# Performance work log

Measured on AMD Instinct MI355X. Metric: run time of the kernel, lower is better.

## Reference

```python
import jax, jax.numpy as jnp
import numpy as np

N = 262144          # ray samples
L = 16              # grid levels
T = 2 ** 19         # hash table entries per level
F = 2               # features per entry
NMIN, NMAX = 16, 2048
SB = 1.0            # scene_bound
DW, CW = 64, 64     # density / color MLP widths

_PRIMES = jnp.array([1, 2654435761, 805459861], dtype=jnp.uint32)
_OFFS = jnp.asarray(np.stack(np.meshgrid([0, 1], [0, 1], [0, 1], indexing='ij'), -1).reshape(8, 3), dtype=jnp.uint32)  # 8 cube corners


def _scalings():
    g = np.exp((np.log(NMAX) - np.log(NMIN)) / (L - 1))
    return jnp.asarray(np.floor(NMIN * g ** np.arange(L)), dtype=jnp.float32)  # (L,)


def hash_encode(pos01, table):
    # pos01: (N,3) in [0,1]; table: (L*T, F)
    scaled = pos01[:, None, :] * _scalings()[None, :, None]        # (N,L,3)
    floor = jnp.floor(scaled)
    frac = scaled - floor                                          # (N,L,3)
    corners = floor.astype(jnp.uint32)[:, :, None, :] + _OFFS[None, None]  # (N,L,8,3)
    h = corners * _PRIMES                                          # uint32 wraparound hashing
    idx = (h[..., 0] ^ h[..., 1] ^ h[..., 2]) % jnp.uint32(T)      # (N,L,8)
    idx = idx.astype(jnp.int32) + (jnp.arange(L, dtype=jnp.int32) * T)[None, :, None]
    feats = table[idx]                                             # (N,L,8,F) gather
    sel = _OFFS.astype(bool)[None, None]                           # (1,1,8,3)
    w = jnp.prod(jnp.where(sel, frac[:, :, None, :], 1.0 - frac[:, :, None, :]), axis=-1)  # (N,L,8)
    out = jnp.einsum('nlcf,nlc->nlf', feats, w)                    # trilinear interp
    return out.reshape(out.shape[0], L * F)                        # (N, 32)


def sh_encode(d):
    # 4th-order real spherical harmonics, 16 components (instant-ngp convention)
    x, y, z = d[..., 0], d[..., 1], d[..., 2]
    xx, yy, zz = x * x, y * y, z * z
    xy, yz, xz = x * y, y * z, x * z
    return jnp.stack([
        jnp.full_like(x, 0.28209479177387814),
        -0.48860251190291987 * y,
        0.48860251190291987 * z,
        -0.48860251190291987 * x,
        1.0925484305920792 * xy,
        -1.0925484305920792 * yz,
        0.94617469575755997 * zz - 0.31539156525252005,
        -1.0925484305920792 * xz,
        0.54627421529603959 * (xx - yy),
        0.59004358992664352 * y * (-3.0 * xx + yy),
        2.8906114426405538 * xy * z,
        0.45704579946446572 * y * (1.0 - 5.0 * zz),
        0.3731763325901154 * z * (5.0 * zz - 3.0),
        0.45704579946446572 * x * (1.0 - 5.0 * zz),
        1.445305721320277 * z * (xx - yy),
        0.59004358992664352 * x * (xx - 3.0 * yy),
    ], axis=-1)  # (N,16)


def setup_inputs() -> dict:
    key = jax.random.key(0)
    ks = jax.random.split(key, 10)
    position = jax.random.uniform(ks[0], (N, 3), jnp.float32, -SB, SB)
    d = jax.random.normal(ks[1], (N, 3), jnp.float32)
    direction = d / jnp.linalg.norm(d, axis=-1, keepdims=True)
    hash_table = jax.random.uniform(ks[2], (L * T, F), jnp.float32, -1e-4, 1e-4)
    def dense(k, fin, fout, std):
        return (jax.random.normal(k, (fin, fout), jnp.float32) * std,
                jnp.zeros((fout,), jnp.float32))
    w1, b1 = dense(ks[3], L * F, DW, 0.01)      # normal() init in source
    w2, b2 = dense(ks[4], DW, 16, 0.01)
    w3, b3 = dense(ks[5], 16 + 16, CW, 0.01)
    w4, b4 = dense(ks[6], CW, CW, 0.01)
    w5, b5 = dense(ks[7], CW, 3, 0.1)           # default lecun-ish scale
    return dict(position=position, direction=direction, hash_table=hash_table,
                w1=w1, b1=b1, w2=w2, b2=b2, w3=w3, b3=b3, w4=w4, b4=b4, w5=w5, b5=b5)


def reference(position, direction, hash_table, w1, b1, w2, b2, w3, b3, w4, b4, w5, b5):
    p = (position + SB) / (2.0 * SB)                 # -> [0,1]
    enc = hash_encode(p, hash_table)                 # (N,32)
    h = jax.nn.relu(enc @ w1 + b1)                   # density MLP
    h = h @ w2 + b2                                  # (N,16)
    density = jnp.exp(h[:, 0:1])                     # exponential_density_activation
    sh = sh_encode(direction)                        # (N,16)
    c = jnp.concatenate([h, sh], axis=-1)            # (N,32)
    c = jax.nn.relu(c @ w3 + b3)
    c = jax.nn.relu(c @ w4 + b4)
    c = c @ w5 + b5
    color = jax.nn.sigmoid(c)                        # high_dynamic_range=False
    return jnp.concatenate([density, color], axis=-1)  # (N,4) drgbs
```

## Files before the change

kernel.cpp:

```cpp
#include <hip/hip_runtime.h>
#include <cmath>

namespace {
constexpr int kN = 262144;
constexpr int kL = 16;
constexpr int kT = 1 << 19;
constexpr unsigned kTMask = kT - 1;
constexpr int kB = 4096;

typedef __attribute__((ext_vector_type(8))) short short8;
typedef __attribute__((ext_vector_type(4))) float f32x4;
typedef __attribute__((ext_vector_type(4))) unsigned short ushort4v;

struct Scales { float s[kL]; };

__device__ __forceinline__ unsigned short f2bf(float f) {
    unsigned u = __builtin_bit_cast(unsigned, f);
    return (unsigned short)((u + 0x7FFFu + ((u >> 16) & 1u)) >> 16);
}

__global__ __launch_bounds__(256) void prep_w(
    const float* __restrict__ w1, const float* __restrict__ w2,
    const float* __restrict__ w3, const float* __restrict__ w4,
    const float* __restrict__ w5, unsigned short* __restrict__ out)
{
    const int i = blockIdx.x * 256 + threadIdx.x;
    const int f = i >> 9;
    const int l = (i >> 3) & 63;
    const int e = i & 7;
    const int cl = l & 15;
    const int kg = l >> 4;
    float v = 0.0f;
    if (f < 4) {
        v = w1[(kg * 8 + e) * 64 + f * 16 + cl];
    } else if (f < 6) {
        const int q = f - 4;
        v = w2[(q * 32 + kg * 8 + e) * 16 + cl];
    } else if (f < 10) {
        v = w3[(kg * 8 + e) * 64 + (f - 6) * 16 + cl];
    } else if (f < 18) {
        const int g = f - 10, q = g >> 2, nt = g & 3;
        v = w4[(q * 32 + kg * 8 + e) * 64 + nt * 16 + cl];
    } else {
        const int q = f - 18;
        v = (cl < 3) ? w5[(q * 32 + kg * 8 + e) * 3 + cl] : 0.0f;
    }
    out[i] = f2bf(v);
}

__global__ __launch_bounds__(256) void bucket_hist(
    const float* __restrict__ pos,
    unsigned short* __restrict__ key,
    unsigned* __restrict__ hist)
{
    const int n = blockIdx.x * 256 + threadIdx.x;
    const float px = (pos[n * 3 + 0] + 1.0f) * 0.5f;
    const float py = (pos[n * 3 + 1] + 1.0f) * 0.5f;
    const float pz = (pos[n * 3 + 2] + 1.0f) * 0.5f;
    const int cx = min(15, (int)(px * 16.0f));
    const int cy = min(15, (int)(py * 16.0f));
    const int cz = min(15, (int)(pz * 16.0f));
    const int k = (cx << 8) | (cy << 4) | cz;
    key[n] = (unsigned short)k;
    atomicAdd(&hist[k], 1u);
}

__global__ __launch_bounds__(1024) void bucket_scan(
    const unsigned* __restrict__ hist,
    unsigned* __restrict__ cursor)
{
    __shared__ unsigned s[1024];
    const int t = threadIdx.x;
    const unsigned v0 = hist[4 * t], v1 = hist[4 * t + 1];
    const unsigned v2 = hist[4 * t + 2], v3 = hist[4 * t + 3];
    const unsigned a0 = v0, a1 = a0 + v1, a2 = a1 + v2, a3 = a2 + v3;
    s[t] = a3;
    __syncthreads();
    for (int off = 1; off < 1024; off <<= 1) {
        unsigned x = 0;
        if (t >= off) x = s[t - off];
        __syncthreads();
        if (t >= off) s[t] += x;
        __syncthreads();
    }
    const unsigned base = (t > 0) ? s[t - 1] : 0u;
    cursor[4 * t]     = base;
    cursor[4 * t + 1] = base + a0;
    cursor[4 * t + 2] = base + a1;
    cursor[4 * t + 3] = base + a2;
}

__global__ __launch_bounds__(256) void bucket_scatter(
    const float* __restrict__ pos, const float* __restrict__ dir,
    const unsigned short* __restrict__ key,
    unsigned* __restrict__ cursor,
    float* __restrict__ spos, float* __restrict__ sdir,
    unsigned* __restrict__ s2o)
{
    const int n = blockIdx.x * 256 + threadIdx.x;
    const unsigned k = key[n];
    const unsigned i = atomicAdd(&cursor[k], 1u);
    s2o[i] = (unsigned)n;
    spos[i * 3 + 0] = pos[n * 3 + 0];
    spos[i * 3 + 1] = pos[n * 3 + 1];
    spos[i * 3 + 2] = pos[n * 3 + 2];
    sdir[i * 3 + 0] = dir[n * 3 + 0];
    sdir[i * 3 + 1] = dir[n * 3 + 1];
    sdir[i * 3 + 2] = dir[n * 3 + 2];
}

__global__ __launch_bounds__(256) void ngp_encode(
    const float* __restrict__ spos,
    const float2* __restrict__ table,
    unsigned* __restrict__ enc,
    Scales sc)
{
    const int bid = blockIdx.x;
    const int l = bid >> 10;
    const int n = ((bid & 1023) << 8) | threadIdx.x;

    const float s = sc.s[l];
    const float2* __restrict__ tl = table + (size_t)l * kT;

    const float px = (spos[n * 3 + 0] + 1.0f) * 0.5f;
    const float py = (spos[n * 3 + 1] + 1.0f) * 0.5f;
    const float pz = (spos[n * 3 + 2] + 1.0f) * 0.5f;
    const float sx = px * s, sy = py * s, sz = pz * s;
    const float fx = floorf(sx), fy = floorf(sy), fz = floorf(sz);
    const float rx = sx - fx, ry = sy - fy, rz = sz - fz;
    const unsigned cx = (unsigned)fx, cy = (unsigned)fy, cz = (unsigned)fz;

    const unsigned hy0 = cy * 2654435761u, hy1 = (cy + 1u) * 2654435761u;
    const unsigned hz0 = cz * 805459861u,  hz1 = (cz + 1u) * 805459861u;

    float4 pr[4];
    float2 ex[4];
    unsigned idx0v[4], hyzv[4];

    #pragma unroll
    for (int j = 0; j < 4; ++j) {
        const unsigned hyz = ((j >> 1) ? hy1 : hy0) ^ ((j & 1) ? hz1 : hz0);
        hyzv[j] = hyz;
        const unsigned idx0 = (cx ^ hyz) & kTMask;
        idx0v[j] = idx0;
        pr[j] = *reinterpret_cast<const float4*>(tl + (idx0 & ~1u));
    }

    if (cx & 1u) {
        const unsigned cx1 = cx + 1u;
        #pragma unroll
        for (int j = 0; j < 4; ++j)
            ex[j] = tl[(cx1 ^ hyzv[j]) & kTMask];
    }

    const bool odd = (cx & 1u) != 0u;
    const float wx0 = 1.0f - rx, wx1 = rx;
    float f0 = 0.f, f1 = 0.f;
    #pragma unroll
    for (int j = 0; j < 4; ++j) {
        const float wyz = ((j >> 1) ? ry : 1.0f - ry) *
                          ((j & 1) ? rz : 1.0f - rz);
        const bool hi = (idx0v[j] & 1u) != 0u;
        const float c0x = hi ? pr[j].z : pr[j].x;
        const float c0y = hi ? pr[j].w : pr[j].y;
        const float c1x = odd ? ex[j].x : (hi ? pr[j].x : pr[j].z);
        const float c1y = odd ? ex[j].y : (hi ? pr[j].y : pr[j].w);
        f0 = fmaf(c0x, wx0 * wyz, f0);
        f1 = fmaf(c0y, wx0 * wyz, f1);
        f0 = fmaf(c1x, wx1 * wyz, f0);
        f1 = fmaf(c1y, wx1 * wyz, f1);
    }
    enc[(size_t)l * kN + n] = (unsigned)f2bf(f0) | ((unsigned)f2bf(f1) << 16);
}

__global__ __launch_bounds__(256) void ngp_mlp_mfma(
    const unsigned* __restrict__ enc,
    const unsigned short* __restrict__ wbf,
    const float* __restrict__ sdir,
    const unsigned* __restrict__ s2o,
    const float* __restrict__ b1, const float* __restrict__ b2,
    const float* __restrict__ b3, const float* __restrict__ b4,
    const float* __restrict__ b5,
    float* __restrict__ out)
{
    __shared__ unsigned short sA[4][4096];
    __shared__ unsigned short sB[4][2048];

    const int tid = threadIdx.x;
    const int wid = tid >> 6;
    const int l   = tid & 63;
    const int cl  = l & 15;
    const int kg  = l >> 4;
    unsigned short* __restrict__ A_ = sA[wid];
    unsigned short* __restrict__ B_ = sB[wid];
    const int gbase = blockIdx.x * 256 + wid * 64;

    {
        const int s = gbase + l;
        const float x = sdir[s * 3 + 0], y = sdir[s * 3 + 1], z = sdir[s * 3 + 2];
        const float xx = x * x, yy = y * y, zz = z * z;
        const float xy = x * y, yz = y * z, xz = x * z;
        float sh[16];
        sh[0] = 0.28209479177387814f;
        sh[1] = -0.48860251190291987f * y;
        sh[2] = 0.48860251190291987f * z;
        sh[3] = -0.48860251190291987f * x;
        sh[4] = 1.0925484305920792f * xy;
        sh[5] = -1.0925484305920792f * yz;
        sh[6] = 0.94617469575755997f * zz - 0.31539156525252005f;
        sh[7] = -1.0925484305920792f * xz;
        sh[8] = 0.54627421529603959f * (xx - yy);
        sh[9] = 0.59004358992664352f * y * (-3.0f * xx + yy);
        sh[10] = 2.8906114426405538f * xy * z;
        sh[11] = 0.45704579946446572f * y * (1.0f - 5.0f * zz);
        sh[12] = 0.3731763325901154f * z * (5.0f * zz - 3.0f);
        sh[13] = 0.45704579946446572f * x * (1.0f - 5.0f * zz);
        sh[14] = 1.445305721320277f * z * (xx - yy);
        sh[15] = 0.59004358992664352f * x * (xx - 3.0f * yy);
        #pragma unroll
        for (int j = 0; j < 16; ++j)
            B_[(l >> 4) * 512 + (16 + j) * 16 + (l & 15)] = f2bf(sh[j]);
    }

    short8 A1[4];
    #pragma unroll
    for (int m = 0; m < 4; ++m) {
        #pragma unroll
        for (int j = 0; j < 4; ++j) {
            const unsigned v = enc[(size_t)(kg * 4 + j) * kN + (gbase + m * 16 + cl)];
            A1[m][2 * j]     = (short)(v & 0xFFFFu);
            A1[m][2 * j + 1] = (short)(v >> 16);
        }
    }
    {
        short8 B1[4];
        #pragma unroll
        for (int nt = 0; nt < 4; ++nt)
            B1[nt] = *reinterpret_cast<const short8*>(&wbf[(size_t)(nt) * 512 + l * 8]);

        f32x4 acc[4][4];
        #pragma unroll
        for (int nt = 0; nt < 4; ++nt) {
            const float bv = b1[nt * 16 + cl];
            #pragma unroll
            for (int m = 0; m < 4; ++m) {
                acc[m][nt][0] = bv; acc[m][nt][1] = bv; acc[m][nt][2] = bv; acc[m][nt][3] = bv;
            }
        }
        #pragma unroll
        for (int m = 0; m < 4; ++m)
            #pragma unroll
            for (int nt = 0; nt < 4; ++nt)
                acc[m][nt] = __builtin_amdgcn_mfma_f32_16x16x32_bf16(A1[m], B1[nt], acc[m][nt], 0, 0, 0);

        #pragma unroll
        for (int m = 0; m < 4; ++m) {
            #pragma unroll
            for (int nt = 0; nt < 4; ++nt) {
                ushort4v pk;
                #pragma unroll
                for (int r = 0; r < 4; ++r) pk[r] = f2bf(fmaxf(acc[m][nt][r], 0.0f));
                *reinterpret_cast<ushort4v*>(&A_[m * 1024 + (nt * 16 + cl) * 16 + kg * 4]) = pk;
            }
        }
    }

    {
        short8 A2[4][2];
        #pragma unroll
        for (int m = 0; m < 4; ++m)
            #pragma unroll
            for (int q = 0; q < 2; ++q)
                #pragma unroll
                for (int e = 0; e < 8; ++e)
                    A2[m][q][e] = (short)A_[m * 1024 + (q * 32 + kg * 8 + e) * 16 + cl];

        short8 B2[2];
        #pragma unroll
        for (int q = 0; q < 2; ++q)
            B2[q] = *reinterpret_cast<const short8*>(&wbf[(size_t)(4 + q) * 512 + l * 8]);

        f32x4 acc[4];
        const float bv = b2[cl];
        #pragma unroll
        for (int m = 0; m < 4; ++m) { acc[m][0] = bv; acc[m][1] = bv; acc[m][2] = bv; acc[m][3] = bv; }
        #pragma unroll
        for (int m = 0; m < 4; ++m)
            #pragma unroll
            for (int q = 0; q < 2; ++q)
                acc[m] = __builtin_amdgcn_mfma_f32_16x16x32_bf16(A2[m][q], B2[q], acc[m], 0, 0, 0);

        #pragma unroll
        for (int m = 0; m < 4; ++m) {
            if (cl == 0) {
                #pragma unroll
                for (int r = 0; r < 4; ++r)
                    out[(size_t)s2o[gbase + m * 16 + kg * 4 + r] * 4 + 0] = expf(acc[m][r]);
            }
            ushort4v pk;
            #pragma unroll
            for (int r = 0; r < 4; ++r) pk[r] = f2bf(acc[m][r]);
            *reinterpret_cast<ushort4v*>(&B_[m * 512 + cl * 16 + kg * 4]) = pk;
        }
    }

    {
        short8 A3[4];
        #pragma unroll
        for (int m = 0; m < 4; ++m)
            #pragma unroll
            for (int e = 0; e < 8; ++e)
                A3[m][e] = (short)B_[m * 512 + (kg * 8 + e) * 16 + cl];

        short8 B3[4];
        #pragma unroll
        for (int nt = 0; nt < 4; ++nt)
            B3[nt] = *reinterpret_cast<const short8*>(&wbf[(size_t)(6 + nt) * 512 + l * 8]);

        f32x4 acc[4][4];
        #pragma unroll
        for (int nt = 0; nt < 4; ++nt) {
            const float bv = b3[nt * 16 + cl];
            #pragma unroll
            for (int m = 0; m < 4; ++m) {
                acc[m][nt][0] = bv; acc[m][nt][1] = bv; acc[m][nt][2] = bv; acc[m][nt][3] = bv;
            }
        }
        #pragma unroll
        for (int m = 0; m < 4; ++m)
            #pragma unroll
            for (int nt = 0; nt < 4; ++nt)
                acc[m][nt] = __builtin_amdgcn_mfma_f32_16x16x32_bf16(A3[m], B3[nt], acc[m][nt], 0, 0, 0);

        #pragma unroll
        for (int m = 0; m < 4; ++m) {
            #pragma unroll
            for (int nt = 0; nt < 4; ++nt) {
                ushort4v pk;
                #pragma unroll
                for (int r = 0; r < 4; ++r) pk[r] = f2bf(fmaxf(acc[m][nt][r], 0.0f));
                *reinterpret_cast<ushort4v*>(&A_[m * 1024 + (nt * 16 + cl) * 16 + kg * 4]) = pk;
            }
        }
    }

    {
        short8 A4[4][2];
        #pragma unroll
        for (int m = 0; m < 4; ++m)
            #pragma unroll
            for (int q = 0; q < 2; ++q)
                #pragma unroll
                for (int e = 0; e < 8; ++e)
                    A4[m][q][e] = (short)A_[m * 1024 + (q * 32 + kg * 8 + e) * 16 + cl];

        short8 B4[2][4];
        #pragma unroll
        for (int q = 0; q < 2; ++q)
            #pragma unroll
            for (int nt = 0; nt < 4; ++nt)
                B4[q][nt] = *reinterpret_cast<const short8*>(&wbf[(size_t)(10 + q * 4 + nt) * 512 + l * 8]);

        f32x4 acc[4][4];
        #pragma unroll
        for (int nt = 0; nt < 4; ++nt) {
            const float bv = b4[nt * 16 + cl];
            #pragma unroll
            for (int m = 0; m < 4; ++m) {
                acc[m][nt][0] = bv; acc[m][nt][1] = bv; acc[m][nt][2] = bv; acc[m][nt][3] = bv;
            }
        }
        #pragma unroll
        for (int m = 0; m < 4; ++m)
            #pragma unroll
            for (int nt = 0; nt < 4; ++nt)
                #pragma unroll
                for (int q = 0; q < 2; ++q)
                    acc[m][nt] = __builtin_amdgcn_mfma_f32_16x16x32_bf16(A4[m][q], B4[q][nt], acc[m][nt], 0, 0, 0);

        #pragma unroll
        for (int m = 0; m < 4; ++m) {
            #pragma unroll
            for (int nt = 0; nt < 4; ++nt) {
                ushort4v pk;
                #pragma unroll
                for (int r = 0; r < 4; ++r) pk[r] = f2bf(fmaxf(acc[m][nt][r], 0.0f));
                *reinterpret_cast<ushort4v*>(&A_[m * 1024 + (nt * 16 + cl) * 16 + kg * 4]) = pk;
            }
        }
    }

    {
        short8 A5[4][2];
        #pragma unroll
        for (int m = 0; m < 4; ++m)
            #pragma unroll
            for (int q = 0; q < 2; ++q)
                #pragma unroll
                for (int e = 0; e < 8; ++e)
                    A5[m][q][e] = (short)A_[m * 1024 + (q * 32 + kg * 8 + e) * 16 + cl];

        short8 B5[2];
        #pragma unroll
        for (int q = 0; q < 2; ++q)
            B5[q] = *reinterpret_cast<const short8*>(&wbf[(size_t)(18 + q) * 512 + l * 8]);

        f32x4 acc[4];
        const float bv = (cl < 3) ? b5[cl] : 0.0f;
        #pragma unroll
        for (int m = 0; m < 4; ++m) { acc[m][0] = bv; acc[m][1] = bv; acc[m][2] = bv; acc[m][3] = bv; }
        #pragma unroll
        for (int m = 0; m < 4; ++m)
            #pragma unroll
            for (int q = 0; q < 2; ++q)
                acc[m] = __builtin_amdgcn_mfma_f32_16x16x32_bf16(A5[m][q], B5[q], acc[m], 0, 0, 0);

        if (cl < 3) {
            #pragma unroll
            for (int m = 0; m < 4; ++m)
                #pragma unroll
                for (int r = 0; r < 4; ++r)
                    out[(size_t)s2o[gbase + m * 16 + kg * 4 + r] * 4 + 1 + cl] =
                        1.0f / (1.0f + expf(-acc[m][r]));
        }
    }
}

}

extern "C" void kernel_launch(void* const* d_in, const int* in_sizes, int n_in,
                              void* d_out, int out_size, void* d_ws, size_t ws_size,
                              hipStream_t stream) {
    (void)in_sizes; (void)n_in; (void)out_size; (void)ws_size;

    Scales sc;
    const double g = exp((log(2048.0) - log(16.0)) / 15.0);
    for (int l = 0; l < kL; ++l) sc.s[l] = (float)floor(16.0 * pow(g, (double)l));

    const float*  pos   = (const float*)d_in[0];
    const float*  dir   = (const float*)d_in[1];
    const float2* table = (const float2*)d_in[2];
    const float *w1 = (const float*)d_in[3],  *b1 = (const float*)d_in[4];
    const float *w2 = (const float*)d_in[5],  *b2 = (const float*)d_in[6];
    const float *w3 = (const float*)d_in[7],  *b3 = (const float*)d_in[8];
    const float *w4 = (const float*)d_in[9],  *b4 = (const float*)d_in[10];
    const float *w5 = (const float*)d_in[11], *b5 = (const float*)d_in[12];
    float* out = (float*)d_out;

    char* ws = (char*)d_ws;
    unsigned short* wbf   = (unsigned short*)(ws);
    unsigned*       hist  = (unsigned*)(ws + 65536);
    unsigned*       cursor= (unsigned*)(ws + 81920);
    unsigned short* key   = (unsigned short*)(ws + 98304);
    unsigned*       s2o   = (unsigned*)(ws + 622592);
    float*          spos  = (float*)(ws + 1671168);
    float*          sdir  = (float*)(ws + 4816896);
    unsigned*       enc   = (unsigned*)(ws + 7962624);

    hipMemsetAsync(hist, 0, kB * sizeof(unsigned), stream);
    prep_w<<<40, 256, 0, stream>>>(w1, w2, w3, w4, w5, wbf);
    bucket_hist<<<kN / 256, 256, 0, stream>>>(pos, key, hist);
    bucket_scan<<<1, 1024, 0, stream>>>(hist, cursor);
    bucket_scatter<<<kN / 256, 256, 0, stream>>>(pos, dir, key, cursor, spos, sdir, s2o);
    ngp_encode<<<kL * 1024, 256, 0, stream>>>(spos, table, enc, sc);
    ngp_mlp_mfma<<<kN / 256, 256, 0, stream>>>(enc, wbf, sdir, s2o,
        b1, b2, b3, b4, b5, out);
}
```

Before: 167.9 us.

## Refine spatial bucketing to 32^3 Morton order and drop sorted direction copy

Spatial bucketing moves from a 16^3 row-major key to a 32^3 Morton-ordered key, so sorted samples are more spatially coherent and hash-table gathers in the encode kernel should hit cache more often. The scan is widened to 32 buckets per thread to cover the larger histogram. The scatter no longer writes a sorted direction array; it writes a float4 position (with the index packed into w) for a single vector load in encode. The MLP kernel gathers directions through s2o instead, which saves scatter traffic but adds an indirect, uncoalesced read.

Measured after the change: 164.9 us. Within noise of the previous version (-1.7%).

```diff
diff --git a/kernel.cpp b/kernel.cpp
--- a/kernel.cpp
+++ b/kernel.cpp
@@ -6,7 +6,7 @@
 constexpr int kL = 16;
 constexpr int kT = 1 << 19;
 constexpr unsigned kTMask = kT - 1;
-constexpr int kB = 4096;
+constexpr int kB = 32768;
 
 typedef __attribute__((ext_vector_type(8))) short short8;
 typedef __attribute__((ext_vector_type(4))) float f32x4;
@@ -17,6 +17,14 @@
 __device__ __forceinline__ unsigned short f2bf(float f) {
     unsigned u = __builtin_bit_cast(unsigned, f);
     return (unsigned short)((u + 0x7FFFu + ((u >> 16) & 1u)) >> 16);
+}
+
+__device__ __forceinline__ unsigned morton5(unsigned x) {
+    x &= 31u;
+    x = (x | (x << 8)) & 0x100Fu;
+    x = (x | (x << 4)) & 0x10C3u;
+    x = (x | (x << 2)) & 0x1249u;
+    return x;
 }
 
 __global__ __launch_bounds__(256) void prep_w(
@@ -57,10 +65,10 @@
     const float px = (pos[n * 3 + 0] + 1.0f) * 0.5f;
     const float py = (pos[n * 3 + 1] + 1.0f) * 0.5f;
     const float pz = (pos[n * 3 + 2] + 1.0f) * 0.5f;
-    const int cx = min(15, (int)(px * 16.0f));
-    const int cy = min(15, (int)(py * 16.0f));
-    const int cz = min(15, (int)(pz * 16.0f));
-    const int k = (cx << 8) | (cy << 4) | cz;
+    const unsigned cx = (unsigned)min(31, (int)(px * 32.0f));
+    const unsigned cy = (unsigned)min(31, (int)(py * 32.0f));
+    const unsigned cz = (unsigned)min(31, (int)(pz * 32.0f));
+    const unsigned k = morton5(cx) | (morton5(cy) << 1) | (morton5(cz) << 2);
     key[n] = (unsigned short)k;
     atomicAdd(&hist[k], 1u);
 }
@@ -71,46 +79,43 @@
 {
     __shared__ unsigned s[1024];
     const int t = threadIdx.x;
-    const unsigned v0 = hist[4 * t], v1 = hist[4 * t + 1];
-    const unsigned v2 = hist[4 * t + 2], v3 = hist[4 * t + 3];
-    const unsigned a0 = v0, a1 = a0 + v1, a2 = a1 + v2, a3 = a2 + v3;
-    s[t] = a3;
+    unsigned sum = 0;
+    #pragma unroll 4
+    for (int i = 0; i < 32; ++i) sum += hist[t * 32 + i];
+    s[t] = sum;
     __syncthreads();
     for (int off = 1; off < 1024; off <<= 1) {
-        unsigned x = 0;
-        if (t >= off) x = s[t - off];
+        unsigned x = (t >= off) ? s[t - off] : 0u;
         __syncthreads();
-        if (t >= off) s[t] += x;
+        s[t] += x;
         __syncthreads();
     }
-    const unsigned base = (t > 0) ? s[t - 1] : 0u;
-    cursor[4 * t]     = base;
-    cursor[4 * t + 1] = base + a0;
-    cursor[4 * t + 2] = base + a1;
-    cursor[4 * t + 3] = base + a2;
+    unsigned base = (t > 0) ? s[t - 1] : 0u;
+    #pragma unroll 4
+    for (int i = 0; i < 32; ++i) {
+        const unsigned h = hist[t * 32 + i];
+        cursor[t * 32 + i] = base;
+        base += h;
+    }
 }
 
 __global__ __launch_bounds__(256) void bucket_scatter(
-    const float* __restrict__ pos, const float* __restrict__ dir,
+    const float* __restrict__ pos,
     const unsigned short* __restrict__ key,
     unsigned* __restrict__ cursor,
-    float* __restrict__ spos, float* __restrict__ sdir,
+    float4* __restrict__ spos4,
     unsigned* __restrict__ s2o)
 {
     const int n = blockIdx.x * 256 + threadIdx.x;
     const unsigned k = key[n];
     const unsigned i = atomicAdd(&cursor[k], 1u);
+    spos4[i] = make_float4(pos[n * 3 + 0], pos[n * 3 + 1], pos[n * 3 + 2],
+                           __uint_as_float((unsigned)n));
     s2o[i] = (unsigned)n;
-    spos[i * 3 + 0] = pos[n * 3 + 0];
-    spos[i * 3 + 1] = pos[n * 3 + 1];
-    spos[i * 3 + 2] = pos[n * 3 + 2];
-    sdir[i * 3 + 0] = dir[n * 3 + 0];
-    sdir[i * 3 + 1] = dir[n * 3 + 1];
-    sdir[i * 3 + 2] = dir[n * 3 + 2];
 }
 
 __global__ __launch_bounds__(256) void ngp_encode(
-    const float* __restrict__ spos,
+    const float4* __restrict__ spos4,
     const float2* __restrict__ table,
     unsigned* __restrict__ enc,
     Scales sc)
@@ -122,9 +127,10 @@
     const float s = sc.s[l];
     const float2* __restrict__ tl = table + (size_t)l * kT;
 
-    const float px = (spos[n * 3 + 0] + 1.0f) * 0.5f;
-    const float py = (spos[n * 3 + 1] + 1.0f) * 0.5f;
-    const float pz = (spos[n * 3 + 2] + 1.0f) * 0.5f;
+    const float4 p4 = spos4[n];
+    const float px = (p4.x + 1.0f) * 0.5f;
+    const float py = (p4.y + 1.0f) * 0.5f;
+    const float pz = (p4.z + 1.0f) * 0.5f;
     const float sx = px * s, sy = py * s, sz = pz * s;
     const float fx = floorf(sx), fy = floorf(sy), fz = floorf(sz);
     const float rx = sx - fx, ry = sy - fy, rz = sz - fz;
@@ -176,7 +182,7 @@
 __global__ __launch_bounds__(256) void ngp_mlp_mfma(
     const unsigned* __restrict__ enc,
     const unsigned short* __restrict__ wbf,
-    const float* __restrict__ sdir,
+    const float* __restrict__ dir,
     const unsigned* __restrict__ s2o,
     const float* __restrict__ b1, const float* __restrict__ b2,
     const float* __restrict__ b3, const float* __restrict__ b4,
@@ -196,8 +202,8 @@
     const int gbase = blockIdx.x * 256 + wid * 64;
 
     {
-        const int s = gbase + l;
-        const float x = sdir[s * 3 + 0], y = sdir[s * 3 + 1], z = sdir[s * 3 + 2];
+        const unsigned n = s2o[gbase + l];
+        const float x = dir[n * 3 + 0], y = dir[n * 3 + 1], z = dir[n * 3 + 2];
         const float xx = x * x, yy = y * y, zz = z * z;
         const float xy = x * y, yz = y * z, xz = x * z;
         float sh[16];
@@ -448,21 +454,20 @@
     float* out = (float*)d_out;
 
     char* ws = (char*)d_ws;
-    unsigned short* wbf   = (unsigned short*)(ws);
-    unsigned*       hist  = (unsigned*)(ws + 65536);
-    unsigned*       cursor= (unsigned*)(ws + 81920);
-    unsigned short* key   = (unsigned short*)(ws + 98304);
-    unsigned*       s2o   = (unsigned*)(ws + 622592);
-    float*          spos  = (float*)(ws + 1671168);
-    float*          sdir  = (float*)(ws + 4816896);
-    unsigned*       enc   = (unsigned*)(ws + 7962624);
+    unsigned short* wbf    = (unsigned short*)(ws);
+    unsigned*       hist   = (unsigned*)(ws + 65536);
+    unsigned*       cursor = (unsigned*)(ws + 196608);
+    unsigned short* key    = (unsigned short*)(ws + 327680);
+    unsigned*       s2o    = (unsigned*)(ws + 851968);
+    float4*         spos4  = (float4*)(ws + 1966080);
+    unsigned*       enc    = (unsigned*)(ws + 6291456);
 
     hipMemsetAsync(hist, 0, kB * sizeof(unsigned), stream);
     prep_w<<<40, 256, 0, stream>>>(w1, w2, w3, w4, w5, wbf);
     bucket_hist<<<kN / 256, 256, 0, stream>>>(pos, key, hist);
     bucket_scan<<<1, 1024, 0, stream>>>(hist, cursor);
-    bucket_scatter<<<kN / 256, 256, 0, stream>>>(pos, dir, key, cursor, spos, sdir, s2o);
-    ngp_encode<<<kL * 1024, 256, 0, stream>>>(spos, table, enc, sc);
-    ngp_mlp_mfma<<<kN / 256, 256, 0, stream>>>(enc, wbf, sdir, s2o,
+    bucket_scatter<<<kN / 256, 256, 0, stream>>>(pos, key, cursor, spos4, s2o);
+    ngp_encode<<<kL * 1024, 256, 0, stream>>>(spos4, table, enc, sc);
+    ngp_mlp_mfma<<<kN / 256, 256, 0, stream>>>(enc, wbf, dir, s2o,
         b1, b2, b3, b4, b5, out);
 }
```
